# Kernel optimization log

Hardware: AMD Instinct MI355X
Metric: run time of the kernel (lower is better)

Reference implementation:

```python
import jax, jax.numpy as jnp
import numpy as np

B, N, DIN, DOUT, H = 4, 2048, 512, 512, 8
HD = DOUT // H


def setup_inputs() -> dict:
    key = jax.random.key(0)
    ks = jax.random.split(key, 8)
    x = jax.random.normal(ks[0], (B, N, DIN), dtype=jnp.float32)
    mask = jax.random.randint(ks[1], (B, 1, N, N), 0, 2, dtype=jnp.int32)
    s = 1.0 / np.sqrt(DIN)
    Wq = jax.random.uniform(ks[2], (DOUT, DIN), jnp.float32, -s, s)
    Wk = jax.random.uniform(ks[3], (DOUT, DIN), jnp.float32, -s, s)
    Wv = jax.random.uniform(ks[4], (DOUT, DIN), jnp.float32, -s, s)
    bq = jax.random.uniform(ks[5], (DOUT,), jnp.float32, -s, s)
    bk = jax.random.uniform(ks[6], (DOUT,), jnp.float32, -s, s)
    bv = jax.random.uniform(ks[7], (DOUT,), jnp.float32, -s, s)
    return {"x": x, "Wq": Wq, "bq": bq, "Wk": Wk, "bk": bk, "Wv": Wv, "bv": bv, "mask": mask}


def reference(x, Wq, bq, Wk, bk, Wv, bv, mask):
    b, n, _ = x.shape
    # torch Linear: y = x @ W.T + b ; split heads -> [b, h, n, hd]
    def proj(W, bias):
        y = jnp.einsum('bnd,od->bno', x, W) + bias
        return y.reshape(b, n, H, HD).transpose(0, 2, 1, 3)
    Q, K, V = proj(Wq, bq), proj(Wk, bk), proj(Wv, bv)
    scores = jnp.einsum('bhnd,bhmd->bhnm', Q, K) / np.sqrt(HD).astype(np.float32)
    scores = jnp.where(mask == 0, jnp.float32(-1e9), scores)
    attn = jax.nn.softmax(scores, axis=-1)
    ctx = jnp.einsum('bhnm,bhmd->bhnd', attn, V)
    ctx = ctx.transpose(0, 2, 1, 3).reshape(b, n, DOUT)
    return jax.nn.elu(ctx)
```

## Files before the change

kernel.cpp:

```cpp
#include <hip/hip_runtime.h>
#include <math.h>
#include <stdint.h>

#define CB 4
#define CN 2048
#define CDIN 512
#define CDOUT 512
#define CH 8
#define CHD 64
#define CM (CB * CN)
#define CBH (CB * CH)
#define NKT (CN / 64)

typedef _Float16 f16x8 __attribute__((ext_vector_type(8)));
typedef _Float16 f16x4 __attribute__((ext_vector_type(4)));
typedef float    f32x4 __attribute__((ext_vector_type(4)));

#define QSCALE 0.1803368801111204f

#define PB_X  2048
#define PB_WQ 2176
#define PB_WK 2304
#define PB_WV 2432
#define PB_MB 3456

__global__ __launch_bounds__(256) void prep_kernel(
    const float* __restrict__ x,  _Float16* __restrict__ xh,
    const float* __restrict__ Wq, _Float16* __restrict__ wqh,
    const float* __restrict__ Wk, _Float16* __restrict__ wkh,
    const float* __restrict__ Wv, _Float16* __restrict__ wvh,
    const int* __restrict__ mask, unsigned long long* __restrict__ mbits)
{
    const int bx = blockIdx.x;
    if (bx >= PB_WV) {
        const int lane = threadIdx.x & 63;
        const int wv   = threadIdx.x >> 6;
        const int wbase = (bx - PB_WV) * 256 + wv * 64;
        unsigned long long myword = 0;
        #pragma unroll 8
        for (int it = 0; it < 64; ++it) {
            int v = mask[(size_t)(wbase + it) * 64 + lane];
            unsigned long long bal = __ballot(v != 0);
            if (lane == it) myword = bal;
        }
        mbits[wbase + lane] = myword;
        return;
    }
    const float* s; _Float16* d; int i;
    if (bx < PB_X)       { s = x;  d = xh;  i = bx * 2048 + threadIdx.x * 8; }
    else if (bx < PB_WQ) { s = Wq; d = wqh; i = (bx - PB_X)  * 2048 + threadIdx.x * 8; }
    else if (bx < PB_WK) { s = Wk; d = wkh; i = (bx - PB_WQ) * 2048 + threadIdx.x * 8; }
    else                 { s = Wv; d = wvh; i = (bx - PB_WK) * 2048 + threadIdx.x * 8; }
    float4 a = *(const float4*)&s[i];
    float4 b = *(const float4*)&s[i + 4];
    f16x8 h = {(_Float16)a.x, (_Float16)a.y, (_Float16)a.z, (_Float16)a.w,
               (_Float16)b.x, (_Float16)b.y, (_Float16)b.z, (_Float16)b.w};
    *(f16x8*)&d[i] = h;
}

__global__ __launch_bounds__(256) void proj_kernel(
    const _Float16* __restrict__ xh,
    const _Float16* __restrict__ Wqh, const float* __restrict__ bq,
    const _Float16* __restrict__ Wkh, const float* __restrict__ bk,
    const _Float16* __restrict__ Wvh, const float* __restrict__ bv,
    _Float16* __restrict__ Qf, _Float16* __restrict__ Kf, _Float16* __restrict__ Vt)
{
    const int z = blockIdx.z;
    const _Float16* W; const float* bias;
    if (z == 0)      { W = Wqh; bias = bq; }
    else if (z == 1) { W = Wkh; bias = bk; }
    else             { W = Wvh; bias = bv; }

    __shared__ _Float16 SM[2 * 128 * 72];

    const int tid  = threadIdx.x;
    const int m0   = blockIdx.x * 128;
    const int o0   = blockIdx.y * 128;
    const int lane = tid & 63, w = tid >> 6;
    const int il   = lane & 15, quad = lane >> 4;
    const int srow = tid >> 3, kc = (tid & 7) * 8;

    f32x4 acc[2][8] = {};
    f16x8 xr[4], wr[4];

    #pragma unroll
    for (int i = 0; i < 4; ++i) {
        xr[i] = *(const f16x8*)&xh[(size_t)(m0 + srow + i * 32) * CDIN + kc];
        wr[i] = *(const f16x8*)&W[(size_t)(o0 + srow + i * 32) * CDIN + kc];
    }

    for (int k0 = 0; k0 < CDIN; k0 += 64) {
        #pragma unroll
        for (int i = 0; i < 4; ++i) {
            *(f16x8*)&SM[(srow + i * 32) * 72 + kc] = xr[i];
            *(f16x8*)&SM[9216 + (srow + i * 32) * 72 + kc] = wr[i];
        }
        __syncthreads();

        if (k0 + 64 < CDIN) {
            #pragma unroll
            for (int i = 0; i < 4; ++i) {
                xr[i] = *(const f16x8*)&xh[(size_t)(m0 + srow + i * 32) * CDIN + k0 + 64 + kc];
                wr[i] = *(const f16x8*)&W[(size_t)(o0 + srow + i * 32) * CDIN + k0 + 64 + kc];
            }
        }

        #pragma unroll
        for (int dh = 0; dh < 2; ++dh) {
            f16x8 X0 = *(const f16x8*)&SM[(w * 32 + il) * 72 + dh * 32 + quad * 8];
            f16x8 X1 = *(const f16x8*)&SM[(w * 32 + 16 + il) * 72 + dh * 32 + quad * 8];
            if (z < 2) {
                #pragma unroll
                for (int s = 0; s < 8; ++s) {
                    f16x8 Wv_ = *(const f16x8*)&SM[9216 + (s * 16 + il) * 72 + dh * 32 + quad * 8];
                    acc[0][s] = __builtin_amdgcn_mfma_f32_16x16x32_f16(Wv_, X0, acc[0][s], 0, 0, 0);
                    acc[1][s] = __builtin_amdgcn_mfma_f32_16x16x32_f16(Wv_, X1, acc[1][s], 0, 0, 0);
                }
            } else {
                #pragma unroll
                for (int s = 0; s < 8; ++s) {
                    f16x8 Wv_ = *(const f16x8*)&SM[9216 + (s * 16 + il) * 72 + dh * 32 + quad * 8];
                    acc[0][s] = __builtin_amdgcn_mfma_f32_16x16x32_f16(X0, Wv_, acc[0][s], 0, 0, 0);
                    acc[1][s] = __builtin_amdgcn_mfma_f32_16x16x32_f16(X1, Wv_, acc[1][s], 0, 0, 0);
                }
            }
        }
        __syncthreads();
    }

    const int b  = m0 / CN;
    const int nb = m0 & (CN - 1);
    if (z < 2) {
        const float sc = (z == 0) ? QSCALE : 1.0f;
        #pragma unroll
        for (int s = 0; s < 8; ++s) {
            #pragma unroll
            for (int mi = 0; mi < 2; ++mi) {
                f16x4 pv;
                #pragma unroll
                for (int r = 0; r < 4; ++r)
                    pv[r] = (_Float16)((acc[mi][s][r] + bias[o0 + s * 16 + quad * 4 + r]) * sc);
                *(f16x4*)&SM[(w * 32 + mi * 16 + il) * 140 + s * 16 + quad * 4] = pv;
            }
        }
    } else {
        #pragma unroll
        for (int s = 0; s < 8; ++s) {
            const float bval = bias[o0 + s * 16 + il];
            #pragma unroll
            for (int mi = 0; mi < 2; ++mi) {
                f16x4 pv = {(_Float16)(acc[mi][s][0] + bval),
                            (_Float16)(acc[mi][s][1] + bval),
                            (_Float16)(acc[mi][s][2] + bval),
                            (_Float16)(acc[mi][s][3] + bval)};
                *(f16x4*)&SM[(s * 16 + il) * 140 + w * 32 + mi * 16 + quad * 4] = pv;
            }
        }
    }
    __syncthreads();

    const int uu   = tid & 127;
    const int hseg = tid >> 7;
    const int bh   = b * CH + (o0 >> 6) + hseg;
    if (z < 2) {
        _Float16* dst = ((z == 0) ? Qf : Kf) + ((size_t)bh * CN + nb) * CHD;
        #pragma unroll
        for (int k = 0; k < 8; ++k) {
            int n = k * 16 + (uu >> 3);
            int d = (uu & 7) * 8;
            *(f16x8*)&dst[(size_t)n * CHD + d] =
                *(const f16x8*)&SM[n * 140 + hseg * 64 + d];
        }
    } else {
        _Float16* dst = Vt + (size_t)bh * CHD * CN + nb;
        #pragma unroll
        for (int k = 0; k < 8; ++k) {
            int d = k * 8 + (uu >> 4);
            int n = (uu & 15) * 8;
            *(f16x8*)&dst[(size_t)d * CN + n] =
                *(const f16x8*)&SM[(hseg * 64 + d) * 140 + n];
        }
    }
}

__global__ __launch_bounds__(512, 4) void attn_kernel(
    const _Float16* __restrict__ Qf, const _Float16* __restrict__ Kf,
    const _Float16* __restrict__ Vt, const unsigned long long* __restrict__ mbits,
    float* __restrict__ out)
{
    __shared__ _Float16 Ks[2][64][72];
    __shared__ _Float16 Vs[2][64][72];
    __shared__ _Float16 Ps[8][16][72];

    const int tid  = threadIdx.x;
    const int q0   = blockIdx.x * 128;
    const int bh   = blockIdx.y;
    const int b    = bh >> 3, h = bh & 7;
    const int lane = tid & 63, w = tid >> 6;
    const int il   = lane & 15, quad = lane >> 4;
    const int srow = tid >> 3, sc0 = (tid & 7) * 8;

    const _Float16* Qb = Qf + (size_t)bh * CN * CHD;
    const _Float16* Kb = Kf + (size_t)bh * CN * CHD;
    const _Float16* Vb = Vt + (size_t)bh * CHD * CN;

    const int qg = q0 + w * 16 + il;
    const unsigned long long* mrow = mbits + ((size_t)b * CN + qg) * NKT;

    f16x8 Qa0 = *(const f16x8*)&Qb[(size_t)qg * CHD + quad * 8];
    f16x8 Qa1 = *(const f16x8*)&Qb[(size_t)qg * CHD + 32 + quad * 8];

    const f16x8 ones = {1.f16, 1.f16, 1.f16, 1.f16, 1.f16, 1.f16, 1.f16, 1.f16};

    f32x4 oacc[4] = {};
    f32x4 lacc = {};

    uint4 kA, vA; unsigned long long mn;
    kA = *(const uint4*)&Kb[(size_t)srow * CHD + sc0];
    vA = *(const uint4*)&Vb[(size_t)srow * CN + sc0];
    mn = mrow[0];
    *(uint4*)&Ks[0][srow][sc0] = kA;
    *(uint4*)&Vs[0][srow][sc0] = vA;
    __syncthreads();

    for (int kt = 0; kt < NKT; ++kt) {
        const int cur = kt & 1;
        const unsigned long long mcur = mn;

        if (kt < NKT - 1) {
            kA = *(const uint4*)&Kb[(size_t)((kt + 1) * 64 + srow) * CHD + sc0];
            vA = *(const uint4*)&Vb[(size_t)srow * CN + (kt + 1) * 64 + sc0];
            mn = mrow[kt + 1];
        }

        f32x4 st[4] = {};
        #pragma unroll
        for (int s = 0; s < 4; ++s) {
            f16x8 A0 = *(const f16x8*)&Ks[cur][s * 16 + il][quad * 8];
            f16x8 A1 = *(const f16x8*)&Ks[cur][s * 16 + il][32 + quad * 8];
            st[s] = __builtin_amdgcn_mfma_f32_16x16x32_f16(A0, Qa0, st[s], 0, 0, 0);
            st[s] = __builtin_amdgcn_mfma_f32_16x16x32_f16(A1, Qa1, st[s], 0, 0, 0);
        }

        const uint32_t mlo = (uint32_t)mcur, mhi = (uint32_t)(mcur >> 32);
        #pragma unroll
        for (int s = 0; s < 4; ++s) {
            const uint32_t mm = (s < 2) ? mlo : mhi;
            const int base = (s & 1) * 16 + quad * 4;
            f16x4 pv;
            #pragma unroll
            for (int r = 0; r < 4; ++r) {
                float sv = ((mm >> (base + r)) & 1u) ? st[s][r] : -1e9f;
                pv[r] = (_Float16)__builtin_amdgcn_exp2f(sv);
            }
            *(f16x4*)&Ps[w][il][s * 16 + quad * 4] = pv;
        }

        f16x8 Pa0 = *(const f16x8*)&Ps[w][il][quad * 8];
        f16x8 Pa1 = *(const f16x8*)&Ps[w][il][32 + quad * 8];
        #pragma unroll
        for (int s = 0; s < 4; ++s) {
            f16x8 B0 = *(const f16x8*)&Vs[cur][s * 16 + il][quad * 8];
            f16x8 B1 = *(const f16x8*)&Vs[cur][s * 16 + il][32 + quad * 8];
            oacc[s] = __builtin_amdgcn_mfma_f32_16x16x32_f16(Pa0, B0, oacc[s], 0, 0, 0);
            oacc[s] = __builtin_amdgcn_mfma_f32_16x16x32_f16(Pa1, B1, oacc[s], 0, 0, 0);
        }
        lacc = __builtin_amdgcn_mfma_f32_16x16x32_f16(Pa0, ones, lacc, 0, 0, 0);
        lacc = __builtin_amdgcn_mfma_f32_16x16x32_f16(Pa1, ones, lacc, 0, 0, 0);

        if (kt < NKT - 1) {
            *(uint4*)&Ks[cur ^ 1][srow][sc0] = kA;
            *(uint4*)&Vs[cur ^ 1][srow][sc0] = vA;
            __syncthreads();
        }
    }

    #pragma unroll
    for (int s = 0; s < 4; ++s) {
        const int d = h * CHD + s * 16 + il;
        #pragma unroll
        for (int r = 0; r < 4; ++r) {
            int n = q0 + w * 16 + quad * 4 + r;
            float c = oacc[s][r] / lacc[r];
            out[((size_t)b * CN + n) * CDOUT + d] = c > 0.f ? c : expm1f(c);
        }
    }
}

extern "C" void kernel_launch(void* const* d_in, const int* in_sizes, int n_in,
                              void* d_out, int out_size, void* d_ws, size_t ws_size,
                              hipStream_t stream) {
    const float* x    = (const float*)d_in[0];
    const float* Wq   = (const float*)d_in[1];
    const float* bq   = (const float*)d_in[2];
    const float* Wk   = (const float*)d_in[3];
    const float* bk   = (const float*)d_in[4];
    const float* Wv   = (const float*)d_in[5];
    const float* bv   = (const float*)d_in[6];
    const int*   mask = (const int*)d_in[7];
    float* out = (float*)d_out;

    const size_t nx = (size_t)CM * CDIN;
    const size_t nw = (size_t)CDOUT * CDIN;
    const size_t nt = (size_t)CBH * CN * CHD;
    _Float16* xh  = (_Float16*)d_ws;
    _Float16* wqh = xh + nx;
    _Float16* wkh = wqh + nw;
    _Float16* wvh = wkh + nw;
    _Float16* Qf  = wvh + nw;
    _Float16* Kf  = Qf + nt;
    _Float16* Vt  = Kf + nt;
    unsigned long long* mbits = (unsigned long long*)(Vt + nt);

    prep_kernel<<<dim3(PB_MB), 256, 0, stream>>>(
        x, xh, Wq, wqh, Wk, wkh, Wv, wvh, mask, mbits);
    proj_kernel<<<dim3(CM / 128, CDOUT / 128, 3), 256, 0, stream>>>(
        xh, wqh, bq, wkh, bk, wvh, bv, Qf, Kf, Vt);
    attn_kernel<<<dim3(CN / 128, CBH), 512, 0, stream>>>(
        Qf, Kf, Vt, mbits, out);
}
```

Before: 211.6 us.

## Use direct global-to-LDS loads with XOR swizzle and transposed mask-bit layout

The proj and attention kernels now stage tiles with global_load_lds, which copies straight into shared memory instead of going through registers. Padded rows are replaced by an XOR-swizzled 64-wide layout so LDS reads avoid bank conflicts. The mask bitmap is re-laid out per key tile and query row so the attention kernel's mask loads coalesce across lanes. In the proj kernel the register prefetch of the next K chunk is dropped, so global loads now sit on the critical path after each barrier, and the direct-to-LDS path depends on the compiler emitting the right waits.

```diff
diff --git a/kernel.cpp b/kernel.cpp
--- a/kernel.cpp
+++ b/kernel.cpp
@@ -17,6 +17,13 @@
 typedef float    f32x4 __attribute__((ext_vector_type(4)));
 
 #define QSCALE 0.1803368801111204f
+
+__device__ __forceinline__ void gl_lds16(const void* g, void* l) {
+    __builtin_amdgcn_global_load_lds(
+        (const __attribute__((address_space(1))) unsigned int*)g,
+        (__attribute__((address_space(3))) unsigned int*)l, 16, 0, 0);
+}
+
 
 #define PB_X  2048
 #define PB_WQ 2176
@@ -34,16 +41,18 @@
     const int bx = blockIdx.x;
     if (bx >= PB_WV) {
         const int lane = threadIdx.x & 63;
-        const int wv   = threadIdx.x >> 6;
-        const int wbase = (bx - PB_WV) * 256 + wv * 64;
+        const int Wi   = (bx - PB_WV) * 4 + (threadIdx.x >> 6);
+        const int b    = Wi >> 10;
+        const int t    = (Wi >> 5) & 31;
+        const int n0   = (Wi & 31) * 64;
         unsigned long long myword = 0;
         #pragma unroll 8
         for (int it = 0; it < 64; ++it) {
-            int v = mask[(size_t)(wbase + it) * 64 + lane];
+            int v = mask[((size_t)(b * CN + n0 + it)) * CN + t * 64 + lane];
             unsigned long long bal = __ballot(v != 0);
             if (lane == it) myword = bal;
         }
-        mbits[wbase + lane] = myword;
+        mbits[((size_t)(b * NKT + t)) * CN + n0 + lane] = myword;
         return;
     }
     const float* s; _Float16* d; int i;
@@ -66,60 +75,48 @@
     _Float16* __restrict__ Qf, _Float16* __restrict__ Kf, _Float16* __restrict__ Vt)
 {
     const int z = blockIdx.z;
-    const _Float16* W; const float* bias;
-    if (z == 0)      { W = Wqh; bias = bq; }
-    else if (z == 1) { W = Wkh; bias = bk; }
-    else             { W = Wvh; bias = bv; }
-
-    __shared__ _Float16 SM[2 * 128 * 72];
+    const _Float16* Wp; const float* bias;
+    if (z == 0)      { Wp = Wqh; bias = bq; }
+    else if (z == 1) { Wp = Wkh; bias = bk; }
+    else             { Wp = Wvh; bias = bv; }
+
+    __shared__ _Float16 SM[18432];
 
     const int tid  = threadIdx.x;
     const int m0   = blockIdx.x * 128;
     const int o0   = blockIdx.y * 128;
     const int lane = tid & 63, w = tid >> 6;
     const int il   = lane & 15, quad = lane >> 4;
-    const int srow = tid >> 3, kc = (tid & 7) * 8;
+    const int rsub = lane >> 3;
+    const int csw  = ((lane & 7) ^ (rsub & 7)) * 8;
 
     f32x4 acc[2][8] = {};
-    f16x8 xr[4], wr[4];
-
-    #pragma unroll
-    for (int i = 0; i < 4; ++i) {
-        xr[i] = *(const f16x8*)&xh[(size_t)(m0 + srow + i * 32) * CDIN + kc];
-        wr[i] = *(const f16x8*)&W[(size_t)(o0 + srow + i * 32) * CDIN + kc];
-    }
 
     for (int k0 = 0; k0 < CDIN; k0 += 64) {
         #pragma unroll
         for (int i = 0; i < 4; ++i) {
-            *(f16x8*)&SM[(srow + i * 32) * 72 + kc] = xr[i];
-            *(f16x8*)&SM[9216 + (srow + i * 32) * 72 + kc] = wr[i];
+            const int r0 = w * 32 + i * 8;
+            gl_lds16(&xh[(size_t)(m0 + r0 + rsub) * CDIN + k0 + csw], &SM[r0 * 64]);
+            gl_lds16(&Wp[(size_t)(o0 + r0 + rsub) * CDIN + k0 + csw], &SM[8192 + r0 * 64]);
         }
         __syncthreads();
 
-        if (k0 + 64 < CDIN) {
-            #pragma unroll
-            for (int i = 0; i < 4; ++i) {
-                xr[i] = *(const f16x8*)&xh[(size_t)(m0 + srow + i * 32) * CDIN + k0 + 64 + kc];
-                wr[i] = *(const f16x8*)&W[(size_t)(o0 + srow + i * 32) * CDIN + k0 + 64 + kc];
-            }
-        }
-
         #pragma unroll
         for (int dh = 0; dh < 2; ++dh) {
-            f16x8 X0 = *(const f16x8*)&SM[(w * 32 + il) * 72 + dh * 32 + quad * 8];
-            f16x8 X1 = *(const f16x8*)&SM[(w * 32 + 16 + il) * 72 + dh * 32 + quad * 8];
+            const int ph = ((dh * 4 + quad) ^ (il & 7)) * 8;
+            f16x8 X0 = *(const f16x8*)&SM[(w * 32 + il) * 64 + ph];
+            f16x8 X1 = *(const f16x8*)&SM[(w * 32 + 16 + il) * 64 + ph];
             if (z < 2) {
                 #pragma unroll
                 for (int s = 0; s < 8; ++s) {
-                    f16x8 Wv_ = *(const f16x8*)&SM[9216 + (s * 16 + il) * 72 + dh * 32 + quad * 8];
+                    f16x8 Wv_ = *(const f16x8*)&SM[8192 + (s * 16 + il) * 64 + ph];
                     acc[0][s] = __builtin_amdgcn_mfma_f32_16x16x32_f16(Wv_, X0, acc[0][s], 0, 0, 0);
                     acc[1][s] = __builtin_amdgcn_mfma_f32_16x16x32_f16(Wv_, X1, acc[1][s], 0, 0, 0);
                 }
             } else {
                 #pragma unroll
                 for (int s = 0; s < 8; ++s) {
-                    f16x8 Wv_ = *(const f16x8*)&SM[9216 + (s * 16 + il) * 72 + dh * 32 + quad * 8];
+                    f16x8 Wv_ = *(const f16x8*)&SM[8192 + (s * 16 + il) * 64 + ph];
                     acc[0][s] = __builtin_amdgcn_mfma_f32_16x16x32_f16(X0, Wv_, acc[0][s], 0, 0, 0);
                     acc[1][s] = __builtin_amdgcn_mfma_f32_16x16x32_f16(X1, Wv_, acc[1][s], 0, 0, 0);
                 }
@@ -188,9 +185,9 @@
     const _Float16* __restrict__ Vt, const unsigned long long* __restrict__ mbits,
     float* __restrict__ out)
 {
-    __shared__ _Float16 Ks[2][64][72];
-    __shared__ _Float16 Vs[2][64][72];
-    __shared__ _Float16 Ps[8][16][72];
+    __shared__ _Float16 Ks[2][64 * 64];
+    __shared__ _Float16 Vs[2][64 * 64];
+    __shared__ _Float16 Ps[8][16 * 64];
 
     const int tid  = threadIdx.x;
     const int q0   = blockIdx.x * 128;
@@ -198,29 +195,30 @@
     const int b    = bh >> 3, h = bh & 7;
     const int lane = tid & 63, w = tid >> 6;
     const int il   = lane & 15, quad = lane >> 4;
-    const int srow = tid >> 3, sc0 = (tid & 7) * 8;
+    const int rsub = lane >> 3;
+    const int csw  = ((lane & 7) ^ (rsub & 7)) * 8;
 
     const _Float16* Qb = Qf + (size_t)bh * CN * CHD;
     const _Float16* Kb = Kf + (size_t)bh * CN * CHD;
     const _Float16* Vb = Vt + (size_t)bh * CHD * CN;
 
     const int qg = q0 + w * 16 + il;
-    const unsigned long long* mrow = mbits + ((size_t)b * CN + qg) * NKT;
+    const unsigned long long* mbb = mbits + (size_t)b * NKT * CN + qg;
 
     f16x8 Qa0 = *(const f16x8*)&Qb[(size_t)qg * CHD + quad * 8];
     f16x8 Qa1 = *(const f16x8*)&Qb[(size_t)qg * CHD + 32 + quad * 8];
 
     const f16x8 ones = {1.f16, 1.f16, 1.f16, 1.f16, 1.f16, 1.f16, 1.f16, 1.f16};
 
+    const int phA0 = ((quad    ) ^ (il & 7)) * 8;
+    const int phA1 = ((quad + 4) ^ (il & 7)) * 8;
+
     f32x4 oacc[4] = {};
     f32x4 lacc = {};
 
-    uint4 kA, vA; unsigned long long mn;
-    kA = *(const uint4*)&Kb[(size_t)srow * CHD + sc0];
-    vA = *(const uint4*)&Vb[(size_t)srow * CN + sc0];
-    mn = mrow[0];
-    *(uint4*)&Ks[0][srow][sc0] = kA;
-    *(uint4*)&Vs[0][srow][sc0] = vA;
+    gl_lds16(&Kb[(size_t)(w * 8 + rsub) * CHD + csw], &Ks[0][w * 8 * 64]);
+    gl_lds16(&Vb[(size_t)(w * 8 + rsub) * CN + csw], &Vs[0][w * 8 * 64]);
+    unsigned long long mn = mbb[0];
     __syncthreads();
 
     for (int kt = 0; kt < NKT; ++kt) {
@@ -228,16 +226,18 @@
         const unsigned long long mcur = mn;
 
         if (kt < NKT - 1) {
-            kA = *(const uint4*)&Kb[(size_t)((kt + 1) * 64 + srow) * CHD + sc0];
-            vA = *(const uint4*)&Vb[(size_t)srow * CN + (kt + 1) * 64 + sc0];
-            mn = mrow[kt + 1];
+            gl_lds16(&Kb[(size_t)((kt + 1) * 64 + w * 8 + rsub) * CHD + csw],
+                     &Ks[cur ^ 1][w * 8 * 64]);
+            gl_lds16(&Vb[(size_t)(w * 8 + rsub) * CN + (kt + 1) * 64 + csw],
+                     &Vs[cur ^ 1][w * 8 * 64]);
+            mn = mbb[(size_t)(kt + 1) * CN];
         }
 
         f32x4 st[4] = {};
         #pragma unroll
         for (int s = 0; s < 4; ++s) {
-            f16x8 A0 = *(const f16x8*)&Ks[cur][s * 16 + il][quad * 8];
-            f16x8 A1 = *(const f16x8*)&Ks[cur][s * 16 + il][32 + quad * 8];
+            f16x8 A0 = *(const f16x8*)&Ks[cur][(s * 16 + il) * 64 + phA0];
+            f16x8 A1 = *(const f16x8*)&Ks[cur][(s * 16 + il) * 64 + phA1];
             st[s] = __builtin_amdgcn_mfma_f32_16x16x32_f16(A0, Qa0, st[s], 0, 0, 0);
             st[s] = __builtin_amdgcn_mfma_f32_16x16x32_f16(A1, Qa1, st[s], 0, 0, 0);
         }
@@ -253,26 +253,23 @@
                 float sv = ((mm >> (base + r)) & 1u) ? st[s][r] : -1e9f;
                 pv[r] = (_Float16)__builtin_amdgcn_exp2f(sv);
             }
-            *(f16x4*)&Ps[w][il][s * 16 + quad * 4] = pv;
-        }
-
-        f16x8 Pa0 = *(const f16x8*)&Ps[w][il][quad * 8];
-        f16x8 Pa1 = *(const f16x8*)&Ps[w][il][32 + quad * 8];
+            *(f16x4*)&Ps[w][il * 64 +
+                (((s * 2 + (quad >> 1)) ^ (il & 7)) << 3) + ((quad & 1) << 2)] = pv;
+        }
+
+        f16x8 Pa0 = *(const f16x8*)&Ps[w][il * 64 + phA0];
+        f16x8 Pa1 = *(const f16x8*)&Ps[w][il * 64 + phA1];
         #pragma unroll
         for (int s = 0; s < 4; ++s) {
-            f16x8 B0 = *(const f16x8*)&Vs[cur][s * 16 + il][quad * 8];
-            f16x8 B1 = *(const f16x8*)&Vs[cur][s * 16 + il][32 + quad * 8];
+            f16x8 B0 = *(const f16x8*)&Vs[cur][(s * 16 + il) * 64 + phA0];
+            f16x8 B1 = *(const f16x8*)&Vs[cur][(s * 16 + il) * 64 + phA1];
             oacc[s] = __builtin_amdgcn_mfma_f32_16x16x32_f16(Pa0, B0, oacc[s], 0, 0, 0);
             oacc[s] = __builtin_amdgcn_mfma_f32_16x16x32_f16(Pa1, B1, oacc[s], 0, 0, 0);
         }
         lacc = __builtin_amdgcn_mfma_f32_16x16x32_f16(Pa0, ones, lacc, 0, 0, 0);
         lacc = __builtin_amdgcn_mfma_f32_16x16x32_f16(Pa1, ones, lacc, 0, 0, 0);
 
-        if (kt < NKT - 1) {
-            *(uint4*)&Ks[cur ^ 1][srow][sc0] = kA;
-            *(uint4*)&Vs[cur ^ 1][srow][sc0] = vA;
-            __syncthreads();
-        }
+        if (kt < NKT - 1) __syncthreads();
     }
 
     #pragma unroll
```

Result: no change. 214.2 us (+1.3%).
